# Performance work log

Hardware: AMD Instinct MI355X
Metric: run time of the kernel (lower is better)

Reference implementation:

```python
import jax, jax.numpy as jnp
import numpy as np

NUM_GROUPS = 32
EPS = 1e-6


def group_norm(x, gamma, beta):
    # x: [B, C, H, W]
    b, c, h, w = x.shape
    xg = x.reshape(b, NUM_GROUPS, c // NUM_GROUPS, h, w)
    mean = xg.mean(axis=(2, 3, 4), keepdims=True)
    var = xg.var(axis=(2, 3, 4), keepdims=True)
    xn = ((xg - mean) * jax.lax.rsqrt(var + EPS)).reshape(b, c, h, w)
    return xn * gamma[None, :, None, None] + beta[None, :, None, None]


def setup_inputs() -> dict:
    key = jax.random.key(0)
    ks = jax.random.split(key, 10)
    B, C, H, W = 2, 512, 64, 64
    s = 1.0 / np.sqrt(C)
    return {
        "x": jax.random.normal(ks[0], (B, C, H, W), dtype=jnp.float32),
        "gamma": jnp.ones((C,), jnp.float32),
        "beta": jnp.zeros((C,), jnp.float32),
        "Wq": jax.random.normal(ks[1], (C, C), jnp.float32) * s,
        "bq": jnp.zeros((C,), jnp.float32),
        "Wk": jax.random.normal(ks[2], (C, C), jnp.float32) * s,
        "bk": jnp.zeros((C,), jnp.float32),
        "Wv": jax.random.normal(ks[3], (C, C), jnp.float32) * s,
        "bv": jnp.zeros((C,), jnp.float32),
        "Wo": jax.random.normal(ks[4], (C, C), jnp.float32) * s,
        "bo": jnp.zeros((C,), jnp.float32),
    }


def reference(x, gamma, beta, Wq, bq, Wk, bk, Wv, bv, Wo, bo):
    b, c, h, w = x.shape
    hn = group_norm(x, gamma, beta)               # [B,C,H,W]
    hf = hn.reshape(b, c, h * w)                  # [B,C,N]
    # 1x1 convs == channel matmuls
    q = jnp.einsum('oc,bcn->bon', Wq, hf) + bq[None, :, None]
    k = jnp.einsum('oc,bcn->bon', Wk, hf) + bk[None, :, None]
    v = jnp.einsum('oc,bcn->bon', Wv, hf) + bv[None, :, None]
    scale = float(c) ** -0.5
    scores = jnp.einsum('bci,bcj->bij', q, k) * scale   # [B,N,N]
    attn = jax.nn.softmax(scores, axis=-1)
    out = jnp.einsum('bij,bcj->bci', attn, v)            # [B,C,N]
    out = jnp.einsum('oc,bcn->bon', Wo, out) + bo[None, :, None]
    return x + out.reshape(b, c, h, w)
```

## Files before the change

kernel.cpp:

```cpp
#include <hip/hip_runtime.h>

#define BB 2
#define CC 512
#define NS 4096
#define NGROUP 32
#define TILE 128
#define RSTRIDE 132

typedef __bf16 bf16_8 __attribute__((ext_vector_type(8)));
typedef __bf16 bf16_4 __attribute__((ext_vector_type(4)));
typedef float f32_4 __attribute__((ext_vector_type(4)));

#define SMEM_BYTES 33792

__device__ __forceinline__ void gld_lds16(const __bf16* g, __bf16* l) {
  __builtin_amdgcn_global_load_lds(
      (const __attribute__((address_space(1))) unsigned int*)g,
      (__attribute__((address_space(3))) unsigned int*)l, 16, 0, 0);
}

__global__ __launch_bounds__(256) void gn_stats(const float* __restrict__ x,
                                                float* __restrict__ stats) {
  const float4* p = (const float4*)(x + (size_t)blockIdx.x * 65536);
  float s = 0.f, q = 0.f;
  for (int i = threadIdx.x; i < 16384; i += 256) {
    float4 v = p[i];
    s += v.x + v.y + v.z + v.w;
    q += v.x * v.x + v.y * v.y + v.z * v.z + v.w * v.w;
  }
#pragma unroll
  for (int off = 32; off > 0; off >>= 1) {
    s += __shfl_down(s, off, 64);
    q += __shfl_down(q, off, 64);
  }
  __shared__ float ls[4], lq[4];
  int wave = threadIdx.x >> 6, lane = threadIdx.x & 63;
  if (lane == 0) { ls[wave] = s; lq[wave] = q; }
  __syncthreads();
  if (threadIdx.x == 0) {
    float S = ls[0] + ls[1] + ls[2] + ls[3];
    float Q = lq[0] + lq[1] + lq[2] + lq[3];
    float mean = S * (1.f / 65536.f);
    float var = Q * (1.f / 65536.f) - mean * mean;
    stats[blockIdx.x * 2] = mean;
    stats[blockIdx.x * 2 + 1] = rsqrtf(var + 1e-6f);
  }
}

__global__ __launch_bounds__(256) void gn_apply_t(const float* __restrict__ x,
                                                  const float* __restrict__ stats,
                                                  const float* __restrict__ gamma,
                                                  const float* __restrict__ beta,
                                                  __bf16* __restrict__ hnT) {
  __shared__ float tile[32][33];
  int b = blockIdx.z;
  int c0 = blockIdx.y * 32;
  int n0 = blockIdx.x * 32;
  int tx = threadIdx.x;
  int ty = threadIdx.y;
  const float* xb = x + (size_t)b * CC * NS;
#pragma unroll
  for (int i = 0; i < 4; i++) {
    int c = c0 + ty + i * 8;
    float mean = stats[(b * NGROUP + (c >> 4)) * 2 + 0];
    float rstd = stats[(b * NGROUP + (c >> 4)) * 2 + 1];
    float v = xb[(size_t)c * NS + n0 + tx];
    tile[ty + i * 8][tx] = (v - mean) * rstd * gamma[c] + beta[c];
  }
  __syncthreads();
  __bf16* out = hnT + (size_t)b * NS * CC;
#pragma unroll
  for (int i = 0; i < 4; i++) {
    int n = n0 + ty + i * 8;
    out[(size_t)n * CC + c0 + tx] = (__bf16)tile[tx][ty + i * 8];
  }
}

__global__ __launch_bounds__(256) void cvt_w(const float* __restrict__ w0, const float* __restrict__ w1,
                                             const float* __restrict__ w2, const float* __restrict__ w3,
                                             __bf16* __restrict__ o0, __bf16* __restrict__ o1,
                                             __bf16* __restrict__ o2, __bf16* __restrict__ o3) {
  int tsel = blockIdx.x >> 8;
  int i = (blockIdx.x & 255) * 256 + threadIdx.x;
  const float* src = tsel == 0 ? w0 : tsel == 1 ? w1 : tsel == 2 ? w2 : w3;
  __bf16* dst = tsel == 0 ? o0 : tsel == 1 ? o1 : tsel == 2 ? o2 : o3;
  float4 v = ((const float4*)src)[i];
  bf16_4 r;
  r[0] = (__bf16)v.x; r[1] = (__bf16)v.y; r[2] = (__bf16)v.z; r[3] = (__bf16)v.w;
  ((bf16_4*)dst)[i] = r;
}

__device__ __forceinline__ void gemm_core8(const __bf16* __restrict__ A, const __bf16* __restrict__ B,
                                           int K, int lda, int ldb,
                                           __bf16* lA, __bf16* lB, f32_4 (&acc)[4][2]) {
  const int t = threadIdx.x;
  const int lane = t & 63;
  const int wave = t >> 6;
  const int lrow = lane & 15, quad = lane >> 4;
  const int wrow = (wave >> 2) * 64, wcol = (wave & 3) * 32;
  const int co = (quad ^ ((lrow >> 1) & 3)) * 8;
  const int r0 = t >> 2;
  const int kp = ((t & 3) ^ ((t >> 3) & 3)) * 8;
  const __bf16* pA = A + (size_t)r0 * lda + kp;
  const __bf16* pB = B + (size_t)r0 * ldb + kp;
  for (int k0 = 0; k0 < K; k0 += 64) {
    __syncthreads();
    gld_lds16(pA + k0,      &lA[t * 8]);
    gld_lds16(pA + k0 + 32, &lA[4096 + t * 8]);
    gld_lds16(pB + k0,      &lB[t * 8]);
    gld_lds16(pB + k0 + 32, &lB[4096 + t * 8]);
    __syncthreads();
#pragma unroll
    for (int ks = 0; ks < 2; ks++) {
      const __bf16* la = lA + ks * 4096;
      const __bf16* lb = lB + ks * 4096;
      bf16_8 af[4], bfr[2];
#pragma unroll
      for (int i = 0; i < 4; i++)
        af[i] = *(const bf16_8*)&la[(wrow + i * 16 + lrow) * 32 + co];
#pragma unroll
      for (int j = 0; j < 2; j++)
        bfr[j] = *(const bf16_8*)&lb[(wcol + j * 16 + lrow) * 32 + co];
#pragma unroll
      for (int i = 0; i < 4; i++)
#pragma unroll
        for (int j = 0; j < 2; j++)
          acc[i][j] = __builtin_amdgcn_mfma_f32_16x16x32_bf16(af[i], bfr[j], acc[i][j], 0, 0, 0);
    }
  }
}

__device__ __forceinline__ void stage_acc8(float* ls, const f32_4 (&acc)[4][2], int pass) {
  const int t = threadIdx.x;
  const int lane = t & 63, wave = t >> 6;
  const int lrow = lane & 15, quad = lane >> 4;
  const int wrow = (wave >> 2) * 64, wcol = (wave & 3) * 32;
  if ((wrow >> 6) == pass) {
#pragma unroll
    for (int i = 0; i < 4; i++)
#pragma unroll
      for (int r = 0; r < 4; r++)
#pragma unroll
        for (int jj = 0; jj < 2; jj++)
          ls[(i * 16 + quad * 4 + r) * RSTRIDE + wcol + jj * 16 + lrow] = acc[i][jj][r];
  }
}

__device__ __forceinline__ void drain_bf16_8(const float* ls, __bf16* gdst, int ldg) {
  const int t = threadIdx.x;
#pragma unroll
  for (int k2 = 0; k2 < 4; k2++) {
    int idx = k2 * 512 + t;
    int row = idx >> 5, col = (idx & 31) * 4;
    f32_4 v = *(const f32_4*)&ls[row * RSTRIDE + col];
    bf16_4 o;
    o[0] = (__bf16)v[0]; o[1] = (__bf16)v[1]; o[2] = (__bf16)v[2]; o[3] = (__bf16)v[3];
    *(bf16_4*)&gdst[(size_t)row * ldg + col] = o;
  }
}

__device__ __forceinline__ void gemm_core4(const __bf16* __restrict__ A, const __bf16* __restrict__ B,
                                           int K, int lda, int ldb,
                                           __bf16* lA, __bf16* lB, f32_4 (&acc)[4][4]) {
  const int t = threadIdx.x;
  const int lane = t & 63;
  const int wave = t >> 6;
  const int lrow = lane & 15, quad = lane >> 4;
  const int wrow = (wave >> 1) * 64, wcol = (wave & 1) * 64;
  const int co = (quad ^ ((lrow >> 1) & 3)) * 8;
  const int r0 = t >> 2;
  const int kp = ((t & 3) ^ ((t >> 3) & 3)) * 8;
  const __bf16* pA0 = A + (size_t)r0 * lda + kp;
  const __bf16* pA1 = A + (size_t)(r0 + 64) * lda + kp;
  const __bf16* pB0 = B + (size_t)r0 * ldb + kp;
  const __bf16* pB1 = B + (size_t)(r0 + 64) * ldb + kp;
  for (int k0 = 0; k0 < K; k0 += 64) {
    __syncthreads();
    gld_lds16(pA0 + k0,      &lA[t * 8]);
    gld_lds16(pA1 + k0,      &lA[2048 + t * 8]);
    gld_lds16(pA0 + k0 + 32, &lA[4096 + t * 8]);
    gld_lds16(pA1 + k0 + 32, &lA[6144 + t * 8]);
    gld_lds16(pB0 + k0,      &lB[t * 8]);
    gld_lds16(pB1 + k0,      &lB[2048 + t * 8]);
    gld_lds16(pB0 + k0 + 32, &lB[4096 + t * 8]);
    gld_lds16(pB1 + k0 + 32, &lB[6144 + t * 8]);
    __syncthreads();
#pragma unroll
    for (int ks = 0; ks < 2; ks++) {
      const __bf16* la = lA + ks * 4096;
      const __bf16* lb = lB + ks * 4096;
      bf16_8 af[4], bfr[4];
#pragma unroll
      for (int i = 0; i < 4; i++)
        af[i] = *(const bf16_8*)&la[(wrow + i * 16 + lrow) * 32 + co];
#pragma unroll
      for (int j = 0; j < 4; j++)
        bfr[j] = *(const bf16_8*)&lb[(wcol + j * 16 + lrow) * 32 + co];
#pragma unroll
      for (int i = 0; i < 4; i++)
#pragma unroll
        for (int j = 0; j < 4; j++)
          acc[i][j] = __builtin_amdgcn_mfma_f32_16x16x32_bf16(af[i], bfr[j], acc[i][j], 0, 0, 0);
    }
  }
}

__global__ __launch_bounds__(512, 4) void qkv_gemm(const __bf16* __restrict__ hnT,
                                                   const __bf16* __restrict__ Wq,
                                                   const __bf16* __restrict__ Wk,
                                                   const __bf16* __restrict__ Wv,
                                                   const float* __restrict__ bq,
                                                   const float* __restrict__ bk,
                                                   const float* __restrict__ bv,
                                                   __bf16* __restrict__ qT,
                                                   __bf16* __restrict__ kT,
                                                   __bf16* __restrict__ vv) {
  __shared__ char smem[SMEM_BYTES];
  __bf16* lA = (__bf16*)smem;
  __bf16* lB = (__bf16*)(smem + 16384);
  float* lsr = (float*)smem;
  const int b = blockIdx.z;
  const int id = blockIdx.x;
  const int sel = id >> 7;
  const int r = id & 127;
  const long long sBNC = (long long)NS * CC;
  const long long sBCN = (long long)CC * NS;

  int m0, n0, N;
  const __bf16 *Ap, *Bp;
  __bf16* Cp;
  const float* bias;
  if (sel < 2) {
    m0 = (r >> 2) * TILE;
    n0 = (r & 3) * TILE;
    Ap = hnT + (size_t)b * sBNC + (size_t)m0 * CC;
    Bp = (sel == 0 ? Wq : Wk) + (size_t)n0 * CC;
    Cp = (sel == 0 ? qT : kT) + (size_t)b * sBNC;
    bias = (sel == 0 ? bq : bk);
    N = CC;
  } else {
    m0 = (r & 3) * TILE;
    n0 = (r >> 2) * TILE;
    Ap = Wv + (size_t)m0 * CC;
    Bp = hnT + (size_t)b * sBNC + (size_t)n0 * CC;
    Cp = vv + (size_t)b * sBCN;
    bias = bv;
    N = NS;
  }

  f32_4 acc[4][2];
#pragma unroll
  for (int i = 0; i < 4; i++)
#pragma unroll
    for (int j = 0; j < 2; j++) acc[i][j] = {0.f, 0.f, 0.f, 0.f};

  gemm_core8(Ap, Bp, CC, CC, CC, lA, lB, acc);

  const int t = threadIdx.x;
  const int lane = t & 63;
  const int lrow = lane & 15, quad = lane >> 4;
  const int wave = t >> 6;
  const int wrow = (wave >> 2) * 64, wcol = (wave & 3) * 32;
#pragma unroll
  for (int i = 0; i < 4; i++)
#pragma unroll
    for (int r2 = 0; r2 < 4; r2++) {
      float rowb = (sel == 2) ? bias[m0 + wrow + i * 16 + quad * 4 + r2] : 0.f;
#pragma unroll
      for (int j = 0; j < 2; j++) {
        float cb = (sel < 2) ? bias[n0 + wcol + j * 16 + lrow] : rowb;
        acc[i][j][r2] += cb;
      }
    }

#pragma unroll
  for (int p = 0; p < 2; p++) {
    __syncthreads();
    stage_acc8(lsr, acc, p);
    __syncthreads();
    drain_bf16_8(lsr, Cp + (size_t)(m0 + p * 64) * N + n0, N);
  }
}

__global__ __launch_bounds__(256) void e_gemm(const __bf16* __restrict__ qT,
                                              const __bf16* __restrict__ kT,
                                              __bf16* __restrict__ E,
                                              float* __restrict__ l,
                                              float scale) {
  __shared__ char smem[32768];
  __bf16* lA = (__bf16*)smem;
  __bf16* lB = (__bf16*)(smem + 16384);
  const int g = blockIdx.x;
  const int j = g & 7;
  const int b = j & 1;
  const int moct = j >> 1;
  const int k = g >> 3;
  const int sc = k >> 6;
  const int rem = k & 63;
  const int m0 = (moct * 8 + (rem >> 3)) * TILE;
  const int n0 = (sc * 8 + (rem & 7)) * TILE;
  const long long sBNC = (long long)NS * CC;
  const long long sBNN = (long long)NS * NS;
  const __bf16* Ap = qT + (size_t)b * sBNC + (size_t)m0 * CC;
  const __bf16* Bp = kT + (size_t)b * sBNC + (size_t)n0 * CC;

  f32_4 acc[4][4];
#pragma unroll
  for (int i = 0; i < 4; i++)
#pragma unroll
    for (int jj = 0; jj < 4; jj++) acc[i][jj] = {0.f, 0.f, 0.f, 0.f};

  gemm_core4(Ap, Bp, CC, CC, CC, lA, lB, acc);

  const int t = threadIdx.x;
  const int lane = t & 63;
  const int lrow = lane & 15, quad = lane >> 4;
  const int wave = t >> 6;
  const int wrow = (wave >> 1) * 64, wcol = (wave & 1) * 64;
  __bf16* Ep = E + (size_t)b * sBNN;
  float* lp = l + (size_t)b * NS;
#pragma unroll
  for (int i = 0; i < 4; i++) {
#pragma unroll
    for (int r = 0; r < 4; r++) {
      int gm = m0 + wrow + i * 16 + quad * 4 + r;
      float rp = 0.f;
#pragma unroll
      for (int jj = 0; jj < 4; jj++) {
        int gn = n0 + wcol + jj * 16 + lrow;
        float ev = __expf(acc[i][jj][r] * scale);
        rp += ev;
        Ep[(size_t)gm * NS + gn] = (__bf16)ev;
      }
      rp += __shfl_down(rp, 8, 16);
      rp += __shfl_down(rp, 4, 16);
      rp += __shfl_down(rp, 2, 16);
      rp += __shfl_down(rp, 1, 16);
      if (lrow == 0) atomicAdd(&lp[gm], rp);
    }
  }
}

__global__ __launch_bounds__(512, 4) void ao_split4(const __bf16* __restrict__ E,
                                                    const __bf16* __restrict__ vv,
                                                    __bf16* __restrict__ p0,
                                                    __bf16* __restrict__ p1,
                                                    __bf16* __restrict__ p2,
                                                    __bf16* __restrict__ p3) {
  __shared__ char smem[SMEM_BYTES];
  __bf16* lA = (__bf16*)smem;
  __bf16* lB = (__bf16*)(smem + 16384);
  float* lsr = (float*)smem;
  const int g = blockIdx.x;
  const int j = g & 7;
  const int b = j & 1;
  const int split = j >> 1;
  const int k = g >> 3;
  const int m0 = (k >> 2) * TILE;
  const int n0 = (k & 3) * TILE;
  const long long sBNN = (long long)NS * NS;
  const long long sBCN = (long long)CC * NS;
  const long long sBNC = (long long)NS * CC;
  const __bf16* Ap = E + (size_t)b * sBNN + (size_t)m0 * NS + (size_t)split * 1024;
  const __bf16* Bp = vv + (size_t)b * sBCN + (size_t)n0 * NS + (size_t)split * 1024;
  __bf16* Cp = (split == 0 ? p0 : split == 1 ? p1 : split == 2 ? p2 : p3) + (size_t)b * sBNC;

  f32_4 acc[4][2];
#pragma unroll
  for (int i = 0; i < 4; i++)
#pragma unroll
    for (int jj = 0; jj < 2; jj++) acc[i][jj] = {0.f, 0.f, 0.f, 0.f};

  gemm_core8(Ap, Bp, 1024, NS, NS, lA, lB, acc);

#pragma unroll
  for (int p = 0; p < 2; p++) {
    __syncthreads();
    stage_acc8(lsr, acc, p);
    __syncthreads();
    drain_bf16_8(lsr, Cp + (size_t)(m0 + p * 64) * CC + n0, CC);
  }
}

__global__ __launch_bounds__(256) void reduce_ao4(const __bf16* __restrict__ p0,
                                                  const __bf16* __restrict__ p1,
                                                  const __bf16* __restrict__ p2,
                                                  const __bf16* __restrict__ p3,
                                                  const float* __restrict__ l,
                                                  __bf16* __restrict__ o) {
  int i = blockIdx.x * 256 + threadIdx.x;
  int row = i >> 6;
  float inv = 1.f / l[row];
  bf16_8 a = ((const bf16_8*)p0)[i];
  bf16_8 c = ((const bf16_8*)p1)[i];
  bf16_8 d = ((const bf16_8*)p2)[i];
  bf16_8 e = ((const bf16_8*)p3)[i];
  bf16_8 r;
#pragma unroll
  for (int k = 0; k < 8; k++)
    r[k] = (__bf16)(((float)a[k] + (float)c[k] + (float)d[k] + (float)e[k]) * inv);
  ((bf16_8*)o)[i] = r;
}

__global__ __launch_bounds__(512, 4) void wo_split(const __bf16* __restrict__ Wo,
                                                   const __bf16* __restrict__ aoT,
                                                   __bf16* __restrict__ pw0,
                                                   __bf16* __restrict__ pw1) {
  __shared__ char smem[SMEM_BYTES];
  __bf16* lA = (__bf16*)smem;
  __bf16* lB = (__bf16*)(smem + 16384);
  float* lsr = (float*)smem;
  const int b = blockIdx.z & 1;
  const int split = blockIdx.z >> 1;
  const int m0 = blockIdx.y * TILE;
  const int n0 = blockIdx.x * TILE;
  const long long sBNC = (long long)NS * CC;
  const long long sBCN = (long long)CC * NS;
  const __bf16* Ap = Wo + (size_t)m0 * CC + (size_t)split * 256;
  const __bf16* Bp = aoT + (size_t)b * sBNC + (size_t)n0 * CC + (size_t)split * 256;
  __bf16* Cp = (split ? pw1 : pw0) + (size_t)b * sBCN;

  f32_4 acc[4][2];
#pragma unroll
  for (int i = 0; i < 4; i++)
#pragma unroll
    for (int j = 0; j < 2; j++) acc[i][j] = {0.f, 0.f, 0.f, 0.f};

  gemm_core8(Ap, Bp, 256, CC, CC, lA, lB, acc);

#pragma unroll
  for (int p = 0; p < 2; p++) {
    __syncthreads();
    stage_acc8(lsr, acc, p);
    __syncthreads();
    drain_bf16_8(lsr, Cp + (size_t)(m0 + p * 64) * NS + n0, NS);
  }
}

__global__ __launch_bounds__(256) void final_out(const __bf16* __restrict__ pw0,
                                                 const __bf16* __restrict__ pw1,
                                                 const float* __restrict__ bo,
                                                 const float* __restrict__ x,
                                                 float* __restrict__ out) {
  int i = blockIdx.x * 256 + threadIdx.x;
  int o = (i >> 10) & (CC - 1);
  float bias = bo[o];
  bf16_4 a = ((const bf16_4*)pw0)[i];
  bf16_4 c = ((const bf16_4*)pw1)[i];
  float4 xr = ((const float4*)x)[i];
  float4 r;
  r.x = (float)a[0] + (float)c[0] + bias + xr.x;
  r.y = (float)a[1] + (float)c[1] + bias + xr.y;
  r.z = (float)a[2] + (float)c[2] + bias + xr.z;
  r.w = (float)a[3] + (float)c[3] + bias + xr.w;
  ((float4*)out)[i] = r;
}

extern "C" void kernel_launch(void* const* d_in, const int* in_sizes, int n_in,
                              void* d_out, int out_size, void* d_ws, size_t ws_size,
                              hipStream_t stream) {
  const float* x = (const float*)d_in[0];
  const float* gamma = (const float*)d_in[1];
  const float* beta = (const float*)d_in[2];
  const float* Wq = (const float*)d_in[3];
  const float* bq = (const float*)d_in[4];
  const float* Wk = (const float*)d_in[5];
  const float* bk = (const float*)d_in[6];
  const float* Wv = (const float*)d_in[7];
  const float* bv = (const float*)d_in[8];
  const float* Wo = (const float*)d_in[9];
  const float* bo = (const float*)d_in[10];
  float* out = (float*)d_out;

  char* ws = (char*)d_ws;
  __bf16* hnT = (__bf16*)(ws + 0);
  __bf16* qT  = (__bf16*)(ws + 8388608);
  __bf16* kT  = (__bf16*)(ws + 16777216);
  __bf16* vv  = (__bf16*)(ws + 25165824);
  __bf16* aoT = (__bf16*)(ws + 33554432);
  __bf16* Eb  = (__bf16*)(ws + 41943040);
  __bf16* pw0 = (__bf16*)(ws + 41943040);
  __bf16* pw1 = (__bf16*)(ws + 50331648);
  __bf16* Wqb = (__bf16*)(ws + 109051904);
  __bf16* Wkb = (__bf16*)(ws + 109576192);
  __bf16* Wvb = (__bf16*)(ws + 110100480);
  __bf16* Wob = (__bf16*)(ws + 110624768);
  float* stats = (float*)(ws + 111149056);
  float* lsum = (float*)(ws + 109051904);
  __bf16* p0 = hnT;
  __bf16* p1 = qT;
  __bf16* p2 = kT;
  __bf16* p3 = aoT;

  const float scale = 0.044194173824159216f;

  cvt_w<<<1024, 256, 0, stream>>>(Wq, Wk, Wv, Wo, Wqb, Wkb, Wvb, Wob);
  gn_stats<<<BB * NGROUP, 256, 0, stream>>>(x, stats);
  gn_apply_t<<<dim3(NS / 32, CC / 32, BB), dim3(32, 8), 0, stream>>>(x, stats, gamma, beta, hnT);

  qkv_gemm<<<dim3(384, 1, BB), 512, 0, stream>>>(hnT, Wqb, Wkb, Wvb, bq, bk, bv, qT, kT, vv);

  hipMemsetAsync(lsum, 0, BB * NS * sizeof(float), stream);
  e_gemm<<<2048, 256, 0, stream>>>(qT, kT, Eb, lsum, scale);

  ao_split4<<<1024, 512, 0, stream>>>(Eb, vv, p0, p1, p2, p3);
  reduce_ao4<<<2048, 256, 0, stream>>>(p0, p1, p2, p3, lsum, aoT);

  wo_split<<<dim3(NS / TILE, CC / TILE, 2 * BB), 512, 0, stream>>>(Wob, aoT, pw0, pw1);
  final_out<<<4096, 256, 0, stream>>>(pw0, pw1, bo, x, out);
}
```

Measured before the change: 258.3 us.

## Double-buffer LDS tiles in GEMM cores to overlap global loads with MFMA

Result: faster. 247.9 us, median of 2 (-4.0%).

```diff
diff --git a/kernel.cpp b/kernel.cpp
--- a/kernel.cpp
+++ b/kernel.cpp
@@ -11,7 +11,7 @@
 typedef __bf16 bf16_4 __attribute__((ext_vector_type(4)));
 typedef float f32_4 __attribute__((ext_vector_type(4)));
 
-#define SMEM_BYTES 33792
+#define SMEM_BYTES 65536
 
 __device__ __forceinline__ void gld_lds16(const __bf16* g, __bf16* l) {
   __builtin_amdgcn_global_load_lds(
@@ -92,7 +92,7 @@
 
 __device__ __forceinline__ void gemm_core8(const __bf16* __restrict__ A, const __bf16* __restrict__ B,
                                            int K, int lda, int ldb,
-                                           __bf16* lA, __bf16* lB, f32_4 (&acc)[4][2]) {
+                                           __bf16* lds, f32_4 (&acc)[4][2]) {
   const int t = threadIdx.x;
   const int lane = t & 63;
   const int wave = t >> 6;
@@ -103,17 +103,31 @@
   const int kp = ((t & 3) ^ ((t >> 3) & 3)) * 8;
   const __bf16* pA = A + (size_t)r0 * lda + kp;
   const __bf16* pB = B + (size_t)r0 * ldb + kp;
-  for (int k0 = 0; k0 < K; k0 += 64) {
-    __syncthreads();
-    gld_lds16(pA + k0,      &lA[t * 8]);
-    gld_lds16(pA + k0 + 32, &lA[4096 + t * 8]);
-    gld_lds16(pB + k0,      &lB[t * 8]);
-    gld_lds16(pB + k0 + 32, &lB[4096 + t * 8]);
-    __syncthreads();
+  {
+    __bf16* lA = lds;
+    __bf16* lB = lds + 8192;
+    gld_lds16(pA,      &lA[t * 8]);
+    gld_lds16(pA + 32, &lA[4096 + t * 8]);
+    gld_lds16(pB,      &lB[t * 8]);
+    gld_lds16(pB + 32, &lB[4096 + t * 8]);
+  }
+  int buf = 0;
+  for (int k0 = 0; k0 < K; k0 += 64, buf ^= 1) {
+    __syncthreads();
+    if (k0 + 64 < K) {
+      __bf16* lA = lds + (buf ^ 1) * 16384;
+      __bf16* lB = lA + 8192;
+      gld_lds16(pA + k0 + 64, &lA[t * 8]);
+      gld_lds16(pA + k0 + 96, &lA[4096 + t * 8]);
+      gld_lds16(pB + k0 + 64, &lB[t * 8]);
+      gld_lds16(pB + k0 + 96, &lB[4096 + t * 8]);
+    }
+    const __bf16* bA = lds + buf * 16384;
+    const __bf16* bB = bA + 8192;
 #pragma unroll
     for (int ks = 0; ks < 2; ks++) {
-      const __bf16* la = lA + ks * 4096;
-      const __bf16* lb = lB + ks * 4096;
+      const __bf16* la = bA + ks * 4096;
+      const __bf16* lb = bB + ks * 4096;
       bf16_8 af[4], bfr[2];
 #pragma unroll
       for (int i = 0; i < 4; i++)
@@ -161,7 +175,7 @@
 
 __device__ __forceinline__ void gemm_core4(const __bf16* __restrict__ A, const __bf16* __restrict__ B,
                                            int K, int lda, int ldb,
-                                           __bf16* lA, __bf16* lB, f32_4 (&acc)[4][4]) {
+                                           __bf16* lds, f32_4 (&acc)[4][4]) {
   const int t = threadIdx.x;
   const int lane = t & 63;
   const int wave = t >> 6;
@@ -174,21 +188,39 @@
   const __bf16* pA1 = A + (size_t)(r0 + 64) * lda + kp;
   const __bf16* pB0 = B + (size_t)r0 * ldb + kp;
   const __bf16* pB1 = B + (size_t)(r0 + 64) * ldb + kp;
-  for (int k0 = 0; k0 < K; k0 += 64) {
-    __syncthreads();
-    gld_lds16(pA0 + k0,      &lA[t * 8]);
-    gld_lds16(pA1 + k0,      &lA[2048 + t * 8]);
-    gld_lds16(pA0 + k0 + 32, &lA[4096 + t * 8]);
-    gld_lds16(pA1 + k0 + 32, &lA[6144 + t * 8]);
-    gld_lds16(pB0 + k0,      &lB[t * 8]);
-    gld_lds16(pB1 + k0,      &lB[2048 + t * 8]);
-    gld_lds16(pB0 + k0 + 32, &lB[4096 + t * 8]);
-    gld_lds16(pB1 + k0 + 32, &lB[6144 + t * 8]);
-    __syncthreads();
+  {
+    __bf16* lA = lds;
+    __bf16* lB = lds + 8192;
+    gld_lds16(pA0,      &lA[t * 8]);
+    gld_lds16(pA1,      &lA[2048 + t * 8]);
+    gld_lds16(pA0 + 32, &lA[4096 + t * 8]);
+    gld_lds16(pA1 + 32, &lA[6144 + t * 8]);
+    gld_lds16(pB0,      &lB[t * 8]);
+    gld_lds16(pB1,      &lB[2048 + t * 8]);
+    gld_lds16(pB0 + 32, &lB[4096 + t * 8]);
+    gld_lds16(pB1 + 32, &lB[6144 + t * 8]);
+  }
+  int buf = 0;
+  for (int k0 = 0; k0 < K; k0 += 64, buf ^= 1) {
+    __syncthreads();
+    if (k0 + 64 < K) {
+      __bf16* lA = lds + (buf ^ 1) * 16384;
+      __bf16* lB = lA + 8192;
+      gld_lds16(pA0 + k0 + 64, &lA[t * 8]);
+      gld_lds16(pA1 + k0 + 64, &lA[2048 + t * 8]);
+      gld_lds16(pA0 + k0 + 96, &lA[4096 + t * 8]);
+      gld_lds16(pA1 + k0 + 96, &lA[6144 + t * 8]);
+      gld_lds16(pB0 + k0 + 64, &lB[t * 8]);
+      gld_lds16(pB1 + k0 + 64, &lB[2048 + t * 8]);
+      gld_lds16(pB0 + k0 + 96, &lB[4096 + t * 8]);
+      gld_lds16(pB1 + k0 + 96, &lB[6144 + t * 8]);
+    }
+    const __bf16* bA = lds + buf * 16384;
+    const __bf16* bB = bA + 8192;
 #pragma unroll
     for (int ks = 0; ks < 2; ks++) {
-      const __bf16* la = lA + ks * 4096;
-      const __bf16* lb = lB + ks * 4096;
+      const __bf16* la = bA + ks * 4096;
+      const __bf16* lb = bB + ks * 4096;
       bf16_8 af[4], bfr[4];
 #pragma unroll
       for (int i = 0; i < 4; i++)
@@ -216,8 +248,7 @@
                                                    __bf16* __restrict__ kT,
                                                    __bf16* __restrict__ vv) {
   __shared__ char smem[SMEM_BYTES];
-  __bf16* lA = (__bf16*)smem;
-  __bf16* lB = (__bf16*)(smem + 16384);
+  __bf16* lds = (__bf16*)smem;
   float* lsr = (float*)smem;
   const int b = blockIdx.z;
   const int id = blockIdx.x;
@@ -254,7 +285,7 @@
 #pragma unroll
     for (int j = 0; j < 2; j++) acc[i][j] = {0.f, 0.f, 0.f, 0.f};
 
-  gemm_core8(Ap, Bp, CC, CC, CC, lA, lB, acc);
+  gemm_core8(Ap, Bp, CC, CC, CC, lds, acc);
 
   const int t = threadIdx.x;
   const int lane = t & 63;
@@ -287,9 +318,8 @@
                                               __bf16* __restrict__ E,
                                               float* __restrict__ l,
                                               float scale) {
-  __shared__ char smem[32768];
-  __bf16* lA = (__bf16*)smem;
-  __bf16* lB = (__bf16*)(smem + 16384);
+  __shared__ char smem[SMEM_BYTES];
+  __bf16* lds = (__bf16*)smem;
   const int g = blockIdx.x;
   const int j = g & 7;
   const int b = j & 1;
@@ -310,7 +340,7 @@
 #pragma unroll
     for (int jj = 0; jj < 4; jj++) acc[i][jj] = {0.f, 0.f, 0.f, 0.f};
 
-  gemm_core4(Ap, Bp, CC, CC, CC, lA, lB, acc);
+  gemm_core4(Ap, Bp, CC, CC, CC, lds, acc);
 
   const int t = threadIdx.x;
   const int lane = t & 63;
@@ -348,8 +378,7 @@
                                                     __bf16* __restrict__ p2,
                                                     __bf16* __restrict__ p3) {
   __shared__ char smem[SMEM_BYTES];
-  __bf16* lA = (__bf16*)smem;
-  __bf16* lB = (__bf16*)(smem + 16384);
+  __bf16* lds = (__bf16*)smem;
   float* lsr = (float*)smem;
   const int g = blockIdx.x;
   const int j = g & 7;
@@ -371,7 +400,7 @@
 #pragma unroll
     for (int jj = 0; jj < 2; jj++) acc[i][jj] = {0.f, 0.f, 0.f, 0.f};
 
-  gemm_core8(Ap, Bp, 1024, NS, NS, lA, lB, acc);
+  gemm_core8(Ap, Bp, 1024, NS, NS, lds, acc);
 
 #pragma unroll
   for (int p = 0; p < 2; p++) {
@@ -407,8 +436,7 @@
                                                    __bf16* __restrict__ pw0,
                                                    __bf16* __restrict__ pw1) {
   __shared__ char smem[SMEM_BYTES];
-  __bf16* lA = (__bf16*)smem;
-  __bf16* lB = (__bf16*)(smem + 16384);
+  __bf16* lds = (__bf16*)smem;
   float* lsr = (float*)smem;
   const int b = blockIdx.z & 1;
   const int split = blockIdx.z >> 1;
@@ -426,7 +454,7 @@
 #pragma unroll
     for (int j = 0; j < 2; j++) acc[i][j] = {0.f, 0.f, 0.f, 0.f};
 
-  gemm_core8(Ap, Bp, 256, CC, CC, lA, lB, acc);
+  gemm_core8(Ap, Bp, 256, CC, CC, lds, acc);
 
 #pragma unroll
   for (int p = 0; p < 2; p++) {
```
